# Performance work log

Hardware: AMD Instinct MI355X
Metric: run time of the kernel (lower is better)

Reference implementation:

```python
import jax, jax.numpy as jnp
import numpy as np
import math
from itertools import combinations_with_replacement

M_MODES = 10      # photonic modes
N_PHOT = 5        # photons in input state [1,0,1,0,...]
HIDDEN = 100      # number of px phase shifters (hidden_dim)
IN_DIM = 784
N_CLASSES = 10
BATCH = 128

# Fock output states with bunching: multisets of N_PHOT modes -> C(14,5)=2002
_STATES = np.array(list(combinations_with_replacement(range(M_MODES), N_PHOT)), dtype=np.int32)  # [S, n] row indices
_FACT = np.array([
    np.prod([math.factorial(int(c)) for c in np.bincount(s, minlength=M_MODES)])
    for s in _STATES
], dtype=np.float32)  # prod t_j! per output state
# Input-state mode columns (occupied modes) and factorial product (=1 since all occupancies are 1)
_IN_COLS = np.array([0, 2, 4, 6, 8], dtype=np.int32)
# Ryser subsets over n=5 rows
_BITS = np.array([[(k >> i) & 1 for i in range(N_PHOT)] for k in range(2 ** N_PHOT)], dtype=np.float32)  # [K, n]
_SIGNS = ((-1.0) ** (N_PHOT - _BITS.sum(axis=1))).astype(np.float32)  # (-1)^n * (-1)^{|S|}


def _rand_unitary(rng, m):
    z = rng.standard_normal((m, m)) + 1j * rng.standard_normal((m, m))
    q, r = np.linalg.qr(z)
    q = q * (np.diag(r) / np.abs(np.diag(r)))
    return q.astype(np.complex64)


def setup_inputs() -> dict:
    rng = np.random.default_rng(0)
    x = jnp.asarray(rng.standard_normal((BATCH, IN_DIM)), dtype=jnp.float32)
    W1 = jnp.asarray(rng.standard_normal((HIDDEN, IN_DIM)) * 0.03, dtype=jnp.float32)
    b1 = jnp.zeros((HIDDEN,), dtype=jnp.float32)
    UL = _rand_unitary(rng, M_MODES)
    UR = _rand_unitary(rng, M_MODES)
    S = _STATES.shape[0]
    W2 = jnp.asarray(rng.standard_normal((N_CLASSES, S)) * 0.02, dtype=jnp.float32)
    b2 = jnp.zeros((N_CLASSES,), dtype=jnp.float32)
    return {
        "x": x, "W1": W1, "b1": b1,
        "wl_re": jnp.asarray(UL.real), "wl_im": jnp.asarray(UL.imag),
        "wr_re": jnp.asarray(UR.real), "wr_im": jnp.asarray(UR.imag),
        "W2": W2, "b2": b2,
    }


def _forward(x, W1, b1, wl_re, wl_im, wr_re, wr_im, W2, b2):
    B = x.shape[0]
    # downscaling linear + sigmoid -> phase-shifter values px in (0,1)
    h = jax.nn.sigmoid(x @ W1.T + b1)  # [B, HIDDEN]
    # phase shifter i sits on mode i % m; commuting phases on a mode sum
    theta = h.reshape(B, HIDDEN // M_MODES, M_MODES).sum(axis=1)  # [B, m]
    WL = (wl_re + 1j * wl_im).astype(jnp.complex64)
    WR = (wr_re + 1j * wr_im).astype(jnp.complex64)
    phase = jnp.exp(1j * theta.astype(jnp.complex64))  # [B, m]
    # total unitary U = WR @ diag(phase) @ WL
    U = jnp.einsum('pq,bq,qr->bpr', WR, phase, WL)  # [B, m, m]
    A = U[:, :, _IN_COLS]  # columns for occupied input modes -> [B, m, n]
    # per output Fock state, take rows (with multiplicity) -> [B, S, n, n]
    Mx = A[:, jnp.asarray(_STATES), :]
    masks = jnp.asarray(_BITS)   # [K, n]
    signs = jnp.asarray(_SIGNS)  # [K]
    # Ryser: perm = (-1)^n sum_S (-1)^{|S|} prod_j (sum_{i in S} M[i,j])
    rs = jnp.einsum('kn,bsnj->bskj', masks, Mx)       # [B, S, K, n]
    p = jnp.prod(rs, axis=-1)                          # [B, S, K]
    perm = jnp.einsum('k,bsk->bs', signs, p)           # [B, S] complex
    amp = perm / jnp.sqrt(jnp.asarray(_FACT))
    prob = amp.real ** 2 + amp.imag ** 2               # boson-sampling output distribution [B, S]
    return prob @ W2.T + b2                            # output Linear [B, N_CLASSES]


def reference(x, W1, b1, wl_re, wl_im, wr_re, wr_im, W2, b2):
    return _forward(x, W1, b1, wl_re, wl_im, wr_re, wr_im, W2, b2)
```

## Files before the change

### kernel.cpp

```cpp
#include <hip/hip_runtime.h>
#include <utility>
#include <math.h>

#define BATCH     128
#define IN_DIM    784
#define HIDDEN    100
#define MM        10
#define NPH       5
#define NSTATES   2002
#define NCLASSES  10

struct StateTbl { unsigned v[NSTATES]; };

constexpr StateTbl make_state_tbl() {
    StateTbl t{};
    int idx = 0;
    for (int a = 0; a < MM; ++a)
    for (int b = a; b < MM; ++b)
    for (int c = b; c < MM; ++c)
    for (int d = c; d < MM; ++d)
    for (int e = d; e < MM; ++e) {
        int cnt[MM] = {};
        cnt[a]++; cnt[b]++; cnt[c]++; cnt[d]++; cnt[e]++;
        int f = 1;
        for (int m = 0; m < MM; ++m) {
            int kf = 1;
            for (int i = 2; i <= cnt[m]; ++i) kf *= i;
            f *= kf;
        }
        t.v[idx++] = (unsigned)a | ((unsigned)b << 4) | ((unsigned)c << 8) |
                     ((unsigned)d << 12) | ((unsigned)e << 16) |
                     ((unsigned)f << 20);
    }
    return t;
}

__device__ const StateTbl STATE_TBL = make_state_tbl();

template <int K>
__device__ __forceinline__ void glynn_step(
    const float (&mr)[5][5], const float (&mi)[5][5],
    float (&cr)[5], float (&ci)[5], float& accr, float& acci)
{
    constexpr int   bit  = (K & 1) ? 0 : ((K & 2) ? 1 : ((K & 4) ? 2 : 3));
    constexpr int   gray = K ^ (K >> 1);
    constexpr int   row  = bit + 1;
    constexpr float s2   = ((gray >> bit) & 1) ? -2.0f : 2.0f;
    constexpr int   pc   = (gray & 1) + ((gray >> 1) & 1) +
                           ((gray >> 2) & 1) + ((gray >> 3) & 1);
    #pragma unroll
    for (int j = 0; j < 5; ++j) {
        cr[j] = fmaf(s2, mr[row][j], cr[j]);
        ci[j] = fmaf(s2, mi[row][j], ci[j]);
    }
    float pr = cr[0], pi = ci[0];
    #pragma unroll
    for (int j = 1; j < 5; ++j) {
        const float nr = pr * cr[j] - pi * ci[j];
        const float ni = pr * ci[j] + pi * cr[j];
        pr = nr; pi = ni;
    }
    if constexpr ((pc & 1) != 0) { accr -= pr; acci -= pi; }
    else                         { accr += pr; acci += pi; }
}

template <int... Ks>
__device__ __forceinline__ void glynn_run(
    std::integer_sequence<int, Ks...>,
    const float (&mr)[5][5], const float (&mi)[5][5],
    float (&cr)[5], float (&ci)[5], float& accr, float& acci)
{
    (glynn_step<Ks + 1>(mr, mi, cr, ci, accr, acci), ...);
}

__global__ __launch_bounds__(512) void qc_fused(
    const float* __restrict__ x, const float* __restrict__ W1,
    const float* __restrict__ b1,
    const float* __restrict__ wl_re, const float* __restrict__ wl_im,
    const float* __restrict__ wr_re, const float* __restrict__ wr_im,
    const float* __restrict__ W2, const float* __restrict__ b2,
    float* __restrict__ out)
{
    __shared__ __align__(16) float xs[IN_DIM];
    __shared__ float  part[400];
    __shared__ float  hs[HIDDEN];
    __shared__ float  phc[MM], phs_[MM];
    __shared__ float  plr[50], pli[50];
    __shared__ float2 a2[50];
    __shared__ float  wsum[8][NCLASSES];

    const int b   = blockIdx.x;
    const int tid = threadIdx.x;

    for (int i = tid; i < IN_DIM; i += 512) xs[i] = x[b * IN_DIM + i];
    __syncthreads();

    if (tid < 400) {
        const int j = tid >> 2, q = tid & 3;
        const float* wr_ = W1 + j * IN_DIM + q * 196;
        const float* xr  = xs + q * 196;
        float4 acc = make_float4(0.f, 0.f, 0.f, 0.f);
        #pragma unroll 7
        for (int i = 0; i < 196; i += 4) {
            float4 w  = *(const float4*)(wr_ + i);
            float4 xv = *(const float4*)(xr + i);
            acc.x += w.x * xv.x; acc.y += w.y * xv.y;
            acc.z += w.z * xv.z; acc.w += w.w * xv.w;
        }
        part[tid] = (acc.x + acc.y) + (acc.z + acc.w);
    }
    __syncthreads();

    if (tid < HIDDEN) {
        float t = (part[4 * tid] + part[4 * tid + 1]) +
                  (part[4 * tid + 2] + part[4 * tid + 3]) + b1[tid];
        hs[tid] = 1.0f / (1.0f + expf(-t));
    }
    __syncthreads();

    if (tid < MM) {
        float th = 0.f;
        #pragma unroll
        for (int g = 0; g < MM; ++g) th += hs[g * MM + tid];
        float sv, cv;
        sincosf(th, &sv, &cv);
        phc[tid] = cv; phs_[tid] = sv;
    }
    __syncthreads();

    if (tid < 50) {
        const int q = tid / 5, c = tid % 5;
        const float lr = wl_re[q * MM + 2 * c], li = wl_im[q * MM + 2 * c];
        plr[tid] = phc[q] * lr - phs_[q] * li;
        pli[tid] = phc[q] * li + phs_[q] * lr;
    }
    __syncthreads();

    if (tid < 50) {
        const int p = tid / 5, c = tid % 5;
        float ar = 0.f, ai = 0.f;
        #pragma unroll
        for (int q = 0; q < MM; ++q) {
            const float rr = wr_re[p * MM + q], ri = wr_im[p * MM + q];
            const float br = plr[q * 5 + c],    bi = pli[q * 5 + c];
            ar += rr * br - ri * bi;
            ai += rr * bi + ri * br;
        }
        a2[tid] = make_float2(ar, ai);
    }
    __syncthreads();

    float cls[NCLASSES] = {0,0,0,0,0,0,0,0,0,0};

    #pragma unroll
    for (int t = 0; t < 4; ++t) {
        const int s = (t << 9) + tid;
        if (s < NSTATES) {
            const unsigned w = STATE_TBL.v[s];

            float mr[5][5], mi[5][5];
            #pragma unroll
            for (int n = 0; n < 5; ++n) {
                const int base = ((w >> (4 * n)) & 15) * 5;
                #pragma unroll
                for (int j = 0; j < 5; ++j) {
                    const float2 e = a2[base + j];
                    mr[n][j] = e.x; mi[n][j] = e.y;
                }
            }

            float cr[5], ci[5];
            #pragma unroll
            for (int j = 0; j < 5; ++j) {
                cr[j] = ((mr[0][j] + mr[1][j]) + (mr[2][j] + mr[3][j])) + mr[4][j];
                ci[j] = ((mi[0][j] + mi[1][j]) + (mi[2][j] + mi[3][j])) + mi[4][j];
            }
            float accr, acci;
            {
                float pr = cr[0], pi = ci[0];
                #pragma unroll
                for (int j = 1; j < 5; ++j) {
                    const float nr = pr * cr[j] - pi * ci[j];
                    const float ni = pr * ci[j] + pi * cr[j];
                    pr = nr; pi = ni;
                }
                accr = pr; acci = pi;
            }
            glynn_run(std::make_integer_sequence<int, 15>{}, mr, mi, cr, ci, accr, acci);

            const float fact = (float)(w >> 20);
            const float prob = (accr * accr + acci * acci) / (256.0f * fact);

            #pragma unroll
            for (int c = 0; c < NCLASSES; ++c)
                cls[c] = fmaf(prob, W2[c * NSTATES + s], cls[c]);
        }
    }

    #pragma unroll
    for (int c = 0; c < NCLASSES; ++c) {
        float v = cls[c];
        #pragma unroll
        for (int off = 32; off > 0; off >>= 1) v += __shfl_down(v, off, 64);
        if ((tid & 63) == 0) wsum[tid >> 6][c] = v;
    }
    __syncthreads();
    if (tid < NCLASSES) {
        float t = 0.f;
        #pragma unroll
        for (int wv = 0; wv < 8; ++wv) t += wsum[wv][tid];
        out[b * NCLASSES + tid] = t + b2[tid];
    }
}

extern "C" void kernel_launch(void* const* d_in, const int* in_sizes, int n_in,
                              void* d_out, int out_size, void* d_ws, size_t ws_size,
                              hipStream_t stream)
{
    const float* x     = (const float*)d_in[0];
    const float* W1    = (const float*)d_in[1];
    const float* b1    = (const float*)d_in[2];
    const float* wl_re = (const float*)d_in[3];
    const float* wl_im = (const float*)d_in[4];
    const float* wr_re = (const float*)d_in[5];
    const float* wr_im = (const float*)d_in[6];
    const float* W2    = (const float*)d_in[7];
    const float* b2    = (const float*)d_in[8];
    float*       out   = (float*)d_out;

    qc_fused<<<BATCH, 512, 0, stream>>>(x, W1, b1, wl_re, wl_im,
                                        wr_re, wr_im, W2, b2, out);
}
```

Measured before the change: 87.47 us.

## Double block size to 1024 threads and stage probabilities in shared memory

Launches 1024 threads per batch block so each thread handles at most two Fock states instead of four. The W1 dot product is split eight ways per hidden unit using float2 loads. Per-state probabilities are now written to shared memory, and the output projection runs as one wavefront per class reading W2 rows in a coalesced way. This replaces the per-thread 10-class accumulation and cross-wave reduction. The cost is an extra barrier, and the 1024-thread launch bound may force register spilling in the unrolled Glynn loop.

```diff
diff --git a/kernel.cpp b/kernel.cpp
--- a/kernel.cpp
+++ b/kernel.cpp
@@ -73,7 +73,7 @@
     (glynn_step<Ks + 1>(mr, mi, cr, ci, accr, acci), ...);
 }
 
-__global__ __launch_bounds__(512) void qc_fused(
+__global__ __launch_bounds__(1024) void qc_fused(
     const float* __restrict__ x, const float* __restrict__ W1,
     const float* __restrict__ b1,
     const float* __restrict__ wl_re, const float* __restrict__ wl_im,
@@ -82,38 +82,38 @@
     float* __restrict__ out)
 {
     __shared__ __align__(16) float xs[IN_DIM];
-    __shared__ float  part[400];
+    __shared__ float  part[800];
     __shared__ float  hs[HIDDEN];
     __shared__ float  phc[MM], phs_[MM];
     __shared__ float  plr[50], pli[50];
     __shared__ float2 a2[50];
-    __shared__ float  wsum[8][NCLASSES];
+    __shared__ float  probs[2048];
 
     const int b   = blockIdx.x;
     const int tid = threadIdx.x;
 
-    for (int i = tid; i < IN_DIM; i += 512) xs[i] = x[b * IN_DIM + i];
-    __syncthreads();
-
-    if (tid < 400) {
-        const int j = tid >> 2, q = tid & 3;
-        const float* wr_ = W1 + j * IN_DIM + q * 196;
-        const float* xr  = xs + q * 196;
-        float4 acc = make_float4(0.f, 0.f, 0.f, 0.f);
+    if (tid < IN_DIM) xs[tid] = x[b * IN_DIM + tid];
+    __syncthreads();
+
+    if (tid < 800) {
+        const int j = tid >> 3, q = tid & 7;
+        const float* wrow = W1 + j * IN_DIM + q * 98;
+        const float* xr   = xs + q * 98;
+        float2 acc = make_float2(0.f, 0.f);
         #pragma unroll 7
-        for (int i = 0; i < 196; i += 4) {
-            float4 w  = *(const float4*)(wr_ + i);
-            float4 xv = *(const float4*)(xr + i);
+        for (int i = 0; i < 98; i += 2) {
+            const float2 w  = *(const float2*)(wrow + i);
+            const float2 xv = *(const float2*)(xr + i);
             acc.x += w.x * xv.x; acc.y += w.y * xv.y;
-            acc.z += w.z * xv.z; acc.w += w.w * xv.w;
-        }
-        part[tid] = (acc.x + acc.y) + (acc.z + acc.w);
+        }
+        part[tid] = acc.x + acc.y;
     }
     __syncthreads();
 
     if (tid < HIDDEN) {
-        float t = (part[4 * tid] + part[4 * tid + 1]) +
-                  (part[4 * tid + 2] + part[4 * tid + 3]) + b1[tid];
+        const float* p = part + 8 * tid;
+        float t = ((p[0] + p[1]) + (p[2] + p[3])) +
+                  ((p[4] + p[5]) + (p[6] + p[7])) + b1[tid];
         hs[tid] = 1.0f / (1.0f + expf(-t));
     }
     __syncthreads();
@@ -150,11 +150,9 @@
     }
     __syncthreads();
 
-    float cls[NCLASSES] = {0,0,0,0,0,0,0,0,0,0};
-
     #pragma unroll
-    for (int t = 0; t < 4; ++t) {
-        const int s = (t << 9) + tid;
+    for (int t = 0; t < 2; ++t) {
+        const int s = (t << 10) + tid;
         if (s < NSTATES) {
             const unsigned w = STATE_TBL.v[s];
 
@@ -189,27 +187,23 @@
             glynn_run(std::make_integer_sequence<int, 15>{}, mr, mi, cr, ci, accr, acci);
 
             const float fact = (float)(w >> 20);
-            const float prob = (accr * accr + acci * acci) / (256.0f * fact);
-
-            #pragma unroll
-            for (int c = 0; c < NCLASSES; ++c)
-                cls[c] = fmaf(prob, W2[c * NSTATES + s], cls[c]);
-        }
-    }
-
-    #pragma unroll
-    for (int c = 0; c < NCLASSES; ++c) {
-        float v = cls[c];
+            probs[s] = (accr * accr + acci * acci) / (256.0f * fact);
+        } else {
+            probs[s] = 0.f;
+        }
+    }
+    __syncthreads();
+
+    const int c    = tid >> 6;
+    const int lane = tid & 63;
+    if (c < NCLASSES) {
+        const float* w2row = W2 + c * NSTATES;
+        float v = 0.f;
+        for (int s = lane; s < NSTATES; s += 64)
+            v = fmaf(probs[s], w2row[s], v);
         #pragma unroll
         for (int off = 32; off > 0; off >>= 1) v += __shfl_down(v, off, 64);
-        if ((tid & 63) == 0) wsum[tid >> 6][c] = v;
-    }
-    __syncthreads();
-    if (tid < NCLASSES) {
-        float t = 0.f;
-        #pragma unroll
-        for (int wv = 0; wv < 8; ++wv) t += wsum[wv][tid];
-        out[b * NCLASSES + tid] = t + b2[tid];
+        if (lane == 0) out[b * NCLASSES + c] = v + b2[c];
     }
 }
 
@@ -228,6 +222,6 @@
     const float* b2    = (const float*)d_in[8];
     float*       out   = (float*)d_out;
 
-    qc_fused<<<BATCH, 512, 0, stream>>>(x, W1, b1, wl_re, wl_im,
-                                        wr_re, wr_im, W2, b2, out);
-}
+    qc_fused<<<BATCH, 1024, 0, stream>>>(x, W1, b1, wl_re, wl_im,
+                                         wr_re, wr_im, W2, b2, out);
+}
```

Result: slower. 95.13 us (+8.8%).
